# Kernel tuning notes

Measured on AMD Instinct MI355X. Metric: run time of the kernel, lower is better.

Reference implementation:

```python
import jax, jax.numpy as jnp
import numpy as np

HEADS = 16
HEAD_DIM = 64
LN_EPS = 1e-5


def setup_inputs() -> dict:
    key = jax.random.key(0)
    k_x, k_q, k_k, k_v = jax.random.split(key, 4)
    B, C, H, W = 32, 640, 32, 32
    inner = HEADS * HEAD_DIM  # 1024
    x = jax.random.normal(k_x, (B, C, H, W), dtype=jnp.float32)
    # nn.Linear(in_dim, inner_dim, bias=False): weight shape [inner, in_dim]
    Wq = jax.random.normal(k_q, (inner, C), dtype=jnp.float32) * 0.02
    Wk = jax.random.normal(k_k, (inner, C), dtype=jnp.float32) * 0.02
    Wv = jax.random.normal(k_v, (inner, C), dtype=jnp.float32) * 0.02
    # out_norm = nn.LayerNorm(head_dim): default init gamma=1, beta=0
    gamma = jnp.ones((HEAD_DIM,), dtype=jnp.float32)
    beta = jnp.zeros((HEAD_DIM,), dtype=jnp.float32)
    return {"x": x, "Wq": Wq, "Wk": Wk, "Wv": Wv, "gamma": gamma, "beta": beta}


def _layernorm(y, gamma, beta):
    mu = jnp.mean(y, axis=-1, keepdims=True)
    var = jnp.mean(jnp.square(y - mu), axis=-1, keepdims=True)
    return (y - mu) * jax.lax.rsqrt(var + LN_EPS) * gamma + beta


def reference(x, Wq, Wk, Wv, gamma, beta):
    B, C, H, W = x.shape
    N = H * W
    scale = HEAD_DIM ** -0.5
    # rearrange 'b c h w -> b (h w) c' (patch_size=1)
    t = x.reshape(B, C, N).transpose(0, 2, 1)  # [B, N, C]
    def proj(Wm):
        p = jnp.einsum('bnc,ec->bne', t, Wm)  # [B, N, inner]
        return p.reshape(B, N, HEADS, HEAD_DIM).transpose(0, 2, 1, 3)  # [B, h, N, d]
    q, k, v = proj(Wq), proj(Wk), proj(Wv)
    qk = jnp.einsum('bhid,bhjd->bhij', q, k)  # [B, h, N, N]
    p_att = jax.nn.softmax(qk * scale, axis=-1)
    out = jnp.einsum('bhij,bhjd->bhid', p_att, v)  # [B, h, N, d]
    out = out.mean(axis=2)  # [B, h, d]
    return _layernorm(out, gamma, beta)
```

## Files before the change

### kernel.cpp

```cpp
#include <hip/hip_runtime.h>
#include <hip/hip_bf16.h>

typedef __bf16 bf16;
typedef __bf16 bf16x8 __attribute__((ext_vector_type(8)));
typedef float f32x4 __attribute__((ext_vector_type(4)));

#define QSCALE 0.18033688011112042f

#define EXP2(x) __builtin_amdgcn_exp2f(x)

__device__ __forceinline__ void load_lds16(const void* gp, void* lp) {
  __builtin_amdgcn_global_load_lds((const __attribute__((address_space(1))) void*)gp,
                                   (__attribute__((address_space(3))) void*)lp, 16, 0, 0);
}

__global__ __launch_bounds__(256) void k_transpose(const float* __restrict__ x,
                                                   bf16* __restrict__ t) {
  __shared__ float tile[64][65];
  const int b = blockIdx.z, c0 = blockIdx.y * 64, n0 = blockIdx.x * 64;
  const int tid = threadIdx.x, lx = tid & 63, ly = tid >> 6;
  const float* xp = x + ((size_t)b * 640 + c0) * 1024 + n0;
#pragma unroll
  for (int i = 0; i < 16; ++i) {
    int c = i * 4 + ly;
    tile[c][lx] = xp[(size_t)c * 1024 + lx];
  }
  __syncthreads();
  bf16* tp = t + ((size_t)b * 1024 + n0) * 640 + c0;
#pragma unroll
  for (int i = 0; i < 16; ++i) {
    int n = i * 4 + ly;
    tp[(size_t)n * 640 + lx] = (bf16)tile[lx][n];
  }
}

__global__ __launch_bounds__(256) void k_castw(const float* __restrict__ w,
                                               bf16* __restrict__ dst, float s) {
  int i = blockIdx.x * 256 + threadIdx.x;
  if (i < 655360) dst[i] = (bf16)(w[i] * s);
}

__global__ __launch_bounds__(256) void k_gemm_qkv(const bf16* __restrict__ A,
                                                  const bf16* __restrict__ Bw,
                                                  bf16* __restrict__ qkv) {
  __shared__ __align__(16) bf16 As[128 * 64];
  __shared__ __align__(16) bf16 Bs[128 * 64];
  const int tid = threadIdx.x;
  const int lane = tid & 63;
  const int w = tid >> 6;
  const int wm = w & 1, wn = w >> 1;
  const int g = lane >> 4, ln = lane & 15;
  const int m0 = blockIdx.x * 128;
  const int n0 = blockIdx.y * 128;

  f32x4 acc[4][4];
#pragma unroll
  for (int i = 0; i < 4; ++i)
#pragma unroll
    for (int j = 0; j < 4; ++j)
#pragma unroll
      for (int r = 0; r < 4; ++r) acc[i][j][r] = 0.f;

  for (int k0 = 0; k0 < 640; k0 += 64) {
#pragma unroll
    for (int it = 0; it < 4; ++it) {
      int c = it * 256 + w * 64 + lane;
      int m = c >> 3;
      int kq = (c & 7) ^ (m & 7);
      load_lds16(A + (size_t)(m0 + m) * 640 + (k0 + kq * 8), As + (size_t)(it * 256 + w * 64) * 8);
      load_lds16(Bw + (size_t)(n0 + m) * 640 + (k0 + kq * 8), Bs + (size_t)(it * 256 + w * 64) * 8);
    }
    __syncthreads();
#pragma unroll
    for (int kk = 0; kk < 2; ++kk) {
      bf16x8 af[4], bfr[4];
#pragma unroll
      for (int mi = 0; mi < 4; ++mi) {
        int m = wm * 64 + mi * 16 + ln;
        int cc = m * 8 + ((kk * 4 + g) ^ (m & 7));
        af[mi] = *(const bf16x8*)(As + cc * 8);
      }
#pragma unroll
      for (int ni = 0; ni < 4; ++ni) {
        int n = wn * 64 + ni * 16 + ln;
        int cc = n * 8 + ((kk * 4 + g) ^ (n & 7));
        bfr[ni] = *(const bf16x8*)(Bs + cc * 8);
      }
#pragma unroll
      for (int mi = 0; mi < 4; ++mi)
#pragma unroll
        for (int ni = 0; ni < 4; ++ni)
          acc[mi][ni] = __builtin_amdgcn_mfma_f32_16x16x32_bf16(af[mi], bfr[ni], acc[mi][ni], 0, 0, 0);
    }
    __syncthreads();
  }

#pragma unroll
  for (int mi = 0; mi < 4; ++mi)
#pragma unroll
    for (int ni = 0; ni < 4; ++ni)
#pragma unroll
      for (int r = 0; r < 4; ++r) {
        int row = m0 + wm * 64 + mi * 16 + g * 4 + r;
        int col = n0 + wn * 64 + ni * 16 + ln;
        int bb = row >> 10, n = row & 1023;
        int which = col >> 10, h = (col >> 6) & 15, d = col & 63;
        qkv[(size_t)which * 33554432 +
            ((((size_t)bb * 16 + h) * 1024 + n) * 64 + d)] = (bf16)acc[mi][ni][r];
      }
}

__global__ __launch_bounds__(256) void k_attn(const bf16* __restrict__ q,
                                              const bf16* __restrict__ kmat,
                                              float* __restrict__ wsum) {
  __shared__ __align__(16) bf16 Ks[2][4096];
  const int idx = blockIdx.x;
  const int xcd = idx & 7;
  const int y = idx >> 3;
  const int it = y & 3;
  const int bh = xcd + ((y >> 2) << 3);
  const int tid = threadIdx.x;
  const int lane = tid & 63;
  const int w = tid >> 6;
  const int g = lane >> 4, ln = lane & 15;
  const bf16* qb = q + (size_t)bh * 65536;
  const bf16* kb = kmat + (size_t)bh * 65536;
  const int i0 = it * 256 + w * 64;

  const f32x4 zf = {0.f, 0.f, 0.f, 0.f};

#define STAGEK(buf, jt)                                                       \
  do {                                                                        \
    _Pragma("unroll") for (int call_ = 0; call_ < 2; ++call_) {               \
      int p_ = w * 128 + call_ * 64 + lane;                                   \
      int j_ = p_ >> 3;                                                       \
      int kq_ = (p_ & 7) ^ (j_ & 7);                                          \
      load_lds16(kb + (size_t)((jt) * 64 + j_) * 64 + kq_ * 8,                \
                 &Ks[buf][(size_t)(w * 128 + call_ * 64) * 8]);               \
    }                                                                         \
  } while (0)

#define KFRAG(buf, ni, kc)                                                    \
  (*(const bf16x8*)(&Ks[buf][(size_t)(((ni) * 16 + ln) * 8 +                  \
                                      (((kc) * 4 + g) ^ (ln & 7))) * 8]))

  bf16x8 qf[4][2];
#pragma unroll
  for (int mi = 0; mi < 4; ++mi)
#pragma unroll
    for (int kc = 0; kc < 2; ++kc)
      qf[mi][kc] = *(const bf16x8*)(qb + (size_t)(i0 + mi * 16 + ln) * 64 + kc * 32 + g * 8);

  float rs[4][4];
#pragma unroll
  for (int mi = 0; mi < 4; ++mi)
#pragma unroll
    for (int r = 0; r < 4; ++r) rs[mi][r] = 0.f;

  STAGEK(0, 0);
  for (int jt = 0; jt < 16; ++jt) {
    const int cur = jt & 1;
    __syncthreads();
    if (jt + 1 < 16) STAGEK(1 - cur, jt + 1);
    bf16x8 kf[4][2];
#pragma unroll
    for (int ni = 0; ni < 4; ++ni)
#pragma unroll
      for (int kc = 0; kc < 2; ++kc) kf[ni][kc] = KFRAG(cur, ni, kc);
#pragma unroll
    for (int mi = 0; mi < 4; ++mi)
#pragma unroll
      for (int ni = 0; ni < 4; ++ni) {
        f32x4 s = __builtin_amdgcn_mfma_f32_16x16x32_bf16(qf[mi][0], kf[ni][0], zf, 0, 0, 0);
        s = __builtin_amdgcn_mfma_f32_16x16x32_bf16(qf[mi][1], kf[ni][1], s, 0, 0, 0);
#pragma unroll
        for (int r = 0; r < 4; ++r) rs[mi][r] += EXP2(s[r]);
      }
  }
  float rinv[4][4];
#pragma unroll
  for (int mi = 0; mi < 4; ++mi)
#pragma unroll
    for (int r = 0; r < 4; ++r) {
      float v = rs[mi][r];
      v += __shfl_xor(v, 1);
      v += __shfl_xor(v, 2);
      v += __shfl_xor(v, 4);
      v += __shfl_xor(v, 8);
      rinv[mi][r] = 1.0f / v;
    }

  STAGEK(0, 0);
  for (int jt = 0; jt < 16; ++jt) {
    const int cur = jt & 1;
    __syncthreads();
    if (jt + 1 < 16) STAGEK(1 - cur, jt + 1);
    bf16x8 kf[4][2];
#pragma unroll
    for (int ni = 0; ni < 4; ++ni)
#pragma unroll
      for (int kc = 0; kc < 2; ++kc) kf[ni][kc] = KFRAG(cur, ni, kc);
    float cs[4] = {0.f, 0.f, 0.f, 0.f};
#pragma unroll
    for (int mi = 0; mi < 4; ++mi)
#pragma unroll
      for (int ni = 0; ni < 4; ++ni) {
        f32x4 s = __builtin_amdgcn_mfma_f32_16x16x32_bf16(qf[mi][0], kf[ni][0], zf, 0, 0, 0);
        s = __builtin_amdgcn_mfma_f32_16x16x32_bf16(qf[mi][1], kf[ni][1], s, 0, 0, 0);
#pragma unroll
        for (int r = 0; r < 4; ++r) cs[ni] += EXP2(s[r]) * rinv[mi][r];
      }
#pragma unroll
    for (int ni = 0; ni < 4; ++ni) {
      float v = cs[ni];
      v += __shfl_xor(v, 16);
      v += __shfl_xor(v, 32);
      if (g == 0) atomicAdd(wsum + (size_t)bh * 1024 + jt * 64 + ni * 16 + ln, v);
    }
  }
#undef STAGEK
#undef KFRAG
}

__global__ __launch_bounds__(256) void k_final(const float* __restrict__ wsum,
                                               const bf16* __restrict__ v,
                                               const float* __restrict__ gamma,
                                               const float* __restrict__ beta,
                                               float* __restrict__ out) {
  const int bh = blockIdx.x;
  const int tid = threadIdx.x;
  const int d = tid & 63, part = tid >> 6;
  const bf16* vb = v + (size_t)bh * 65536;
  const float* wb = wsum + (size_t)bh * 1024;
  float acc = 0.f;
  for (int j = part * 256; j < part * 256 + 256; ++j)
    acc += wb[j] * (float)vb[(size_t)j * 64 + d];
  __shared__ float red[4][64];
  red[part][d] = acc;
  __syncthreads();
  if (tid < 64) {
    float y = (red[0][d] + red[1][d] + red[2][d] + red[3][d]) * (1.0f / 1024.0f);
    float s1 = y;
#pragma unroll
    for (int off = 1; off < 64; off <<= 1) s1 += __shfl_xor(s1, off);
    float mu = s1 * (1.0f / 64.0f);
    float dy = y - mu;
    float s2 = dy * dy;
#pragma unroll
    for (int off = 1; off < 64; off <<= 1) s2 += __shfl_xor(s2, off);
    float rstd = rsqrtf(s2 * (1.0f / 64.0f) + 1e-5f);
    out[(size_t)bh * 64 + d] = dy * rstd * gamma[d] + beta[d];
  }
}

extern "C" void kernel_launch(void* const* d_in, const int* in_sizes, int n_in,
                              void* d_out, int out_size, void* d_ws, size_t ws_size,
                              hipStream_t stream) {
  const float* x     = (const float*)d_in[0];
  const float* Wq    = (const float*)d_in[1];
  const float* Wk    = (const float*)d_in[2];
  const float* Wv    = (const float*)d_in[3];
  const float* gamma = (const float*)d_in[4];
  const float* beta  = (const float*)d_in[5];
  float* out = (float*)d_out;

  char* ws = (char*)d_ws;
  bf16*  tbf  = (bf16*)ws;
  bf16*  wbf  = (bf16*)(ws + 41943040);
  bf16*  qkv  = (bf16*)(ws + 45875200);
  float* wsum = (float*)(ws + 247201792);

  hipMemsetAsync(wsum, 0, (size_t)512 * 1024 * sizeof(float), stream);
  k_transpose<<<dim3(16, 10, 32), 256, 0, stream>>>(x, tbf);
  k_castw<<<2560, 256, 0, stream>>>(Wq, wbf, QSCALE);
  k_castw<<<2560, 256, 0, stream>>>(Wk, wbf + 655360, 1.0f);
  k_castw<<<2560, 256, 0, stream>>>(Wv, wbf + 1310720, 1.0f);
  k_gemm_qkv<<<dim3(256, 24), 256, 0, stream>>>(tbf, wbf, qkv);
  k_attn<<<2048, 256, 0, stream>>>(qkv, qkv + 33554432, wsum);
  k_final<<<512, 256, 0, stream>>>(wsum, qkv + 67108864, gamma, beta, out);
}
```

Before: 518.4 us.

## Double-buffer QKV GEMM loads, stage epilogue via LDS, merge weight casts

```diff
diff --git a/kernel.cpp b/kernel.cpp
--- a/kernel.cpp
+++ b/kernel.cpp
@@ -34,17 +34,20 @@
   }
 }
 
-__global__ __launch_bounds__(256) void k_castw(const float* __restrict__ w,
-                                               bf16* __restrict__ dst, float s) {
+__global__ __launch_bounds__(256) void k_castw3(const float* __restrict__ wq,
+                                                const float* __restrict__ wk,
+                                                const float* __restrict__ wv,
+                                                bf16* __restrict__ dst) {
   int i = blockIdx.x * 256 + threadIdx.x;
-  if (i < 655360) dst[i] = (bf16)(w[i] * s);
+  if (i < 655360) dst[i] = (bf16)(wq[i] * QSCALE);
+  else if (i < 1310720) dst[i] = (bf16)wk[i - 655360];
+  else if (i < 1966080) dst[i] = (bf16)wv[i - 1310720];
 }
 
 __global__ __launch_bounds__(256) void k_gemm_qkv(const bf16* __restrict__ A,
                                                   const bf16* __restrict__ Bw,
                                                   bf16* __restrict__ qkv) {
-  __shared__ __align__(16) bf16 As[128 * 64];
-  __shared__ __align__(16) bf16 Bs[128 * 64];
+  __shared__ __align__(16) bf16 smem[2][2][8192];
   const int tid = threadIdx.x;
   const int lane = tid & 63;
   const int w = tid >> 6;
@@ -61,16 +64,26 @@
 #pragma unroll
       for (int r = 0; r < 4; ++r) acc[i][j][r] = 0.f;
 
-  for (int k0 = 0; k0 < 640; k0 += 64) {
-#pragma unroll
-    for (int it = 0; it < 4; ++it) {
-      int c = it * 256 + w * 64 + lane;
-      int m = c >> 3;
-      int kq = (c & 7) ^ (m & 7);
-      load_lds16(A + (size_t)(m0 + m) * 640 + (k0 + kq * 8), As + (size_t)(it * 256 + w * 64) * 8);
-      load_lds16(Bw + (size_t)(n0 + m) * 640 + (k0 + kq * 8), Bs + (size_t)(it * 256 + w * 64) * 8);
-    }
+#define GSTAGE(buf, kt)                                                        \
+  do {                                                                         \
+    _Pragma("unroll") for (int it_ = 0; it_ < 4; ++it_) {                      \
+      int c_ = it_ * 256 + w * 64 + lane;                                      \
+      int m_ = c_ >> 3;                                                        \
+      int kq_ = (c_ & 7) ^ (m_ & 7);                                           \
+      load_lds16(A + (size_t)(m0 + m_) * 640 + ((kt) * 64 + kq_ * 8),          \
+                 &smem[buf][0][(size_t)(it_ * 256 + w * 64) * 8]);             \
+      load_lds16(Bw + (size_t)(n0 + m_) * 640 + ((kt) * 64 + kq_ * 8),        \
+                 &smem[buf][1][(size_t)(it_ * 256 + w * 64) * 8]);             \
+    }                                                                          \
+  } while (0)
+
+  GSTAGE(0, 0);
+  for (int kt = 0; kt < 10; ++kt) {
+    const int cur = kt & 1;
     __syncthreads();
+    if (kt + 1 < 10) GSTAGE(1 - cur, kt + 1);
+    const bf16* As = smem[cur][0];
+    const bf16* Bs = smem[cur][1];
 #pragma unroll
     for (int kk = 0; kk < 2; ++kk) {
       bf16x8 af[4], bfr[4];
@@ -92,22 +105,36 @@
         for (int ni = 0; ni < 4; ++ni)
           acc[mi][ni] = __builtin_amdgcn_mfma_f32_16x16x32_bf16(af[mi], bfr[ni], acc[mi][ni], 0, 0, 0);
     }
-    __syncthreads();
-  }
-
+  }
+#undef GSTAGE
+
+  __syncthreads();
+  bf16* ct = &smem[0][0][0];
 #pragma unroll
   for (int mi = 0; mi < 4; ++mi)
 #pragma unroll
     for (int ni = 0; ni < 4; ++ni)
 #pragma unroll
       for (int r = 0; r < 4; ++r) {
-        int row = m0 + wm * 64 + mi * 16 + g * 4 + r;
-        int col = n0 + wn * 64 + ni * 16 + ln;
-        int bb = row >> 10, n = row & 1023;
-        int which = col >> 10, h = (col >> 6) & 15, d = col & 63;
-        qkv[(size_t)which * 33554432 +
-            ((((size_t)bb * 16 + h) * 1024 + n) * 64 + d)] = (bf16)acc[mi][ni][r];
-      }
+        int row = wm * 64 + mi * 16 + g * 4 + r;
+        int col = wn * 64 + ni * 16 + ln;
+        ct[row * 136 + col] = (bf16)acc[mi][ni][r];
+      }
+  __syncthreads();
+  const int which = n0 >> 10;
+  const int hbase = (n0 >> 6) & 15;
+#pragma unroll
+  for (int p = 0; p < 8; ++p) {
+    int row = p * 16 + (tid >> 4);
+    int chunk = tid & 15;
+    bf16x8 vv = *(const bf16x8*)(ct + row * 136 + chunk * 8);
+    int gr = m0 + row;
+    int bb = gr >> 10, n = gr & 1023;
+    int h = hbase + (chunk >> 3);
+    int d0 = (chunk & 7) * 8;
+    *(bf16x8*)(qkv + (size_t)which * 33554432 +
+               (((size_t)bb * 16 + h) * 1024 + n) * 64 + d0) = vv;
+  }
 }
 
 __global__ __launch_bounds__(256) void k_attn(const bf16* __restrict__ q,
@@ -272,9 +299,7 @@
 
   hipMemsetAsync(wsum, 0, (size_t)512 * 1024 * sizeof(float), stream);
   k_transpose<<<dim3(16, 10, 32), 256, 0, stream>>>(x, tbf);
-  k_castw<<<2560, 256, 0, stream>>>(Wq, wbf, QSCALE);
-  k_castw<<<2560, 256, 0, stream>>>(Wk, wbf + 655360, 1.0f);
-  k_castw<<<2560, 256, 0, stream>>>(Wv, wbf + 1310720, 1.0f);
+  k_castw3<<<7680, 256, 0, stream>>>(Wq, Wk, Wv, wbf);
   k_gemm_qkv<<<dim3(256, 24), 256, 0, stream>>>(tbf, wbf, qkv);
   k_attn<<<2048, 256, 0, stream>>>(qkv, qkv + 33554432, wsum);
   k_final<<<512, 256, 0, stream>>>(wsum, qkv + 67108864, gamma, beta, out);
```

Result: no change. 513.1 us (-1.0%).
